# Kernel optimization log

Hardware: AMD Instinct MI355X
Metric: run time of the kernel (lower is better)

The kernel has to match this reference:

```python
import jax, jax.numpy as jnp
import numpy as np

N_HEAD = 16


def setup_inputs() -> dict:
    key = jax.random.key(0)
    ks = jax.random.split(key, 6)
    B, T, H = 4, 2048, 1024
    inp = jax.random.normal(ks[0], (B, T, H), dtype=jnp.float32)
    # padding mask: valid prefix of random length in [T//2, T] per batch row
    lengths = jax.random.randint(ks[1], (B, 1), T // 2, T + 1)
    mask = jnp.arange(T)[None, :] < lengths  # (B, T) bool
    s = 0.02
    w_qkv = jax.random.normal(ks[2], (H, 3 * H), dtype=jnp.float32) * s
    b_qkv = jax.random.normal(ks[3], (3 * H,), dtype=jnp.float32) * s
    w_out = jax.random.normal(ks[4], (H, H), dtype=jnp.float32) * s
    b_out = jax.random.normal(ks[5], (H,), dtype=jnp.float32) * s
    return {"input": inp, "mask": mask, "w_qkv": w_qkv, "b_qkv": b_qkv,
            "w_out": w_out, "b_out": b_out}


def reference(input, mask, w_qkv, b_qkv, w_out, b_out):
    B, T, H = input.shape
    hd = H // N_HEAD
    qkv = input @ w_qkv + b_qkv                       # (B, T, 3H)
    q, k, v = jnp.split(qkv, 3, axis=-1)
    # (B, T, H) -> (B, nh, T, hd)
    q = q.reshape(B, T, N_HEAD, hd).transpose(0, 2, 1, 3)
    k = k.reshape(B, T, N_HEAD, hd).transpose(0, 2, 1, 3)
    v = v.reshape(B, T, N_HEAD, hd).transpose(0, 2, 1, 3)
    scores = jnp.einsum('bhqd,bhkd->bhqk', q, k) / jnp.sqrt(jnp.float32(hd))
    causal = jnp.tril(jnp.ones((T, T), dtype=bool))   # (T, T)
    full_mask = causal[None, None, :, :] & mask[:, None, None, :]  # (B,1,T,T) bcast over heads
    scores = jnp.where(full_mask, scores, -jnp.inf)
    attn = jax.nn.softmax(scores, axis=-1)            # (B, nh, T, T)
    o = jnp.einsum('bhqk,bhkd->bhqd', attn, v)        # (B, nh, T, hd)
    o = o.transpose(0, 2, 1, 3).reshape(B, T, H)
    return o @ w_out + b_out
```

## Files before the change

kernel.cpp:

```cpp
#include <hip/hip_runtime.h>
#include <math.h>

#define B_  4
#define T_  2048
#define H_  1024
#define NH  16
#define HD  64
#define H3  3072

typedef short bf16x8 __attribute__((ext_vector_type(8)));
typedef short bf16x4 __attribute__((ext_vector_type(4)));
typedef float f32x4  __attribute__((ext_vector_type(4)));
typedef float f32x16 __attribute__((ext_vector_type(16)));

#define SC2F 0.18033688011112042f

__device__ __forceinline__ unsigned short f2bf(float f) {
    union { float f; unsigned u; } v; v.f = f;
    unsigned u = v.u;
    unsigned r = (u + 0x7fffu + ((u >> 16) & 1u)) >> 16;
    return (unsigned short)r;
}

__device__ __forceinline__ void gload_lds16(const void* g, void* l) {
    __builtin_amdgcn_global_load_lds(
        (const __attribute__((address_space(1))) unsigned*)g,
        (__attribute__((address_space(3))) unsigned*)l, 16, 0, 0);
}

__device__ __forceinline__ f32x4 mfma_16x16x16_bf16(bf16x4 a, bf16x4 b, f32x4 c) {
#if __has_builtin(__builtin_amdgcn_mfma_f32_16x16x16_bf16)
    return __builtin_amdgcn_mfma_f32_16x16x16_bf16(a, b, c, 0, 0, 0);
#elif __has_builtin(__builtin_amdgcn_mfma_f32_16x16x16bf16_1k)
    return __builtin_amdgcn_mfma_f32_16x16x16bf16_1k(a, b, c, 0, 0, 0);
#else
    f32x4 d;
    asm volatile("v_mfma_f32_16x16x16_bf16 %0, %1, %2, %3"
                 : "=v"(d) : "v"(a), "v"(b), "v"(c));
    return d;
#endif
}

__global__ __launch_bounds__(256) void prep_kernel(
    const float* __restrict__ X, unsigned short* __restrict__ Xbf,
    const float* __restrict__ Wqkv, unsigned short* __restrict__ WqkvT,
    const float* __restrict__ Wout, unsigned short* __restrict__ WoutT)
{
    int bid = blockIdx.x;
    int t = threadIdx.x;
    if (bid < 4096) {
        __shared__ unsigned short tile[32][33];
        int bxx = bid & 127, byy = bid >> 7;
        const float* in;
        unsigned short* out;
        int N, nb;
        if (bxx < 96) { in = Wqkv; out = WqkvT; N = H3; nb = bxx * 32; }
        else          { in = Wout; out = WoutT; N = H_; nb = (bxx - 96) * 32; }
        int kb = byy * 32;
        int tx = t & 31, ty = t >> 5;
        for (int i = 0; i < 32; i += 8)
            tile[ty + i][tx] = f2bf(in[(long)(kb + ty + i) * N + nb + tx]);
        __syncthreads();
        for (int i = 0; i < 32; i += 8)
            out[(long)(nb + ty + i) * H_ + kb + tx] = tile[tx][ty + i];
    } else {
        long u = (long)(bid - 4096) * 256 + t;
#pragma unroll
        for (int j = 0; j < 4; j++) {
            long i = (u + (long)j * 524288) * 4;
            float4 v = *(const float4*)(X + i);
            ushort4 o;
            o.x = f2bf(v.x); o.y = f2bf(v.y); o.z = f2bf(v.z); o.w = f2bf(v.w);
            *(ushort4*)(Xbf + i) = o;
        }
    }
}

__global__ __launch_bounds__(256, 5) void gemm_qkv_kernel(
    const unsigned short* __restrict__ A,
    const unsigned short* __restrict__ Bt,
    const float* __restrict__ bias,
    unsigned short* __restrict__ C,
    unsigned short* __restrict__ Vt)
{
    const int K = H_, N = H3;
    __shared__ unsigned short Asm[128][64];
    __shared__ unsigned short Bsm[128][64];

    int tn = blockIdx.x * 128, tm = blockIdx.y * 128;
    int tid = threadIdx.x;
    int wid = tid >> 6, lane = tid & 63;
    int l31 = lane & 31, lh = lane >> 5;
    int wm = (wid & 1) * 64, wn = (wid >> 1) * 64;

    int rl = lane >> 3;
    int g8 = ((lane & 7) ^ rl) * 8;
    const unsigned short* aP = A  + (long)(tm + wid * 32 + rl) * K + g8;
    const unsigned short* bP = Bt + (long)(tn + wid * 32 + rl) * K + g8;
    int rk = l31 & 7;

    f32x16 acc[2][2] = {};

    for (int k0 = 0; k0 < K; k0 += 64) {
        __syncthreads();
#pragma unroll
        for (int t = 0; t < 4; t++)
            gload_lds16(aP + (long)(t * 8) * K + k0, &Asm[wid * 32 + t * 8][0]);
#pragma unroll
        for (int t = 0; t < 4; t++)
            gload_lds16(bP + (long)(t * 8) * K + k0, &Bsm[wid * 32 + t * 8][0]);
        __syncthreads();

#pragma unroll
        for (int ks = 0; ks < 4; ks++) {
            int pc = ((ks * 2 + lh) ^ rk) * 8;
            bf16x8 af[2], bv[2];
            af[0] = *(const bf16x8*)(&Asm[wm + l31][pc]);
            af[1] = *(const bf16x8*)(&Asm[wm + 32 + l31][pc]);
            bv[0] = *(const bf16x8*)(&Bsm[wn + l31][pc]);
            bv[1] = *(const bf16x8*)(&Bsm[wn + 32 + l31][pc]);
#pragma unroll
            for (int i = 0; i < 2; i++)
#pragma unroll
                for (int j = 0; j < 2; j++)
                    acc[i][j] = __builtin_amdgcn_mfma_f32_32x32x16_bf16(
                        af[i], bv[j], acc[i][j], 0, 0, 0);
        }
    }

    if (tn >= 2 * H_) {
#pragma unroll
        for (int i = 0; i < 2; i++)
#pragma unroll
            for (int j = 0; j < 2; j++) {
                int col = tn + wn + j * 32 + l31;
                float bs = bias[col];
                int feat = col - 2 * H_;
#pragma unroll
                for (int rg = 0; rg < 4; rg++) {
                    int tok0 = tm + wm + i * 32 + rg * 8 + lh * 4;
                    int bb = tok0 >> 11;
                    unsigned d0 = (unsigned)f2bf(acc[i][j][rg * 4 + 0] + bs) |
                                  ((unsigned)f2bf(acc[i][j][rg * 4 + 1] + bs) << 16);
                    unsigned d1 = (unsigned)f2bf(acc[i][j][rg * 4 + 2] + bs) |
                                  ((unsigned)f2bf(acc[i][j][rg * 4 + 3] + bs) << 16);
                    unsigned short* dst = Vt + ((long)(bb * 1024 + feat)) * T_ + (tok0 & (T_ - 1));
                    *(uint2*)dst = make_uint2(d0, d1);
                }
            }
        return;
    }

#pragma unroll
    for (int i = 0; i < 2; i++)
#pragma unroll
        for (int j = 0; j < 2; j++) {
            int col = tn + wn + j * 32 + l31;
            float bs = bias[col];
            bool ks_ = (col >= H_) && (col < 2 * H_);
#pragma unroll
            for (int r = 0; r < 16; r++) {
                int row = tm + wm + i * 32 + (r & 3) + 8 * (r >> 2) + 4 * lh;
                float v = acc[i][j][r] + bs;
                if (ks_) v *= SC2F;
                C[(long)row * N + col] = f2bf(v);
            }
        }
}

template <int TN>
__global__ __launch_bounds__(256) void gemm_kernel(
    const unsigned short* __restrict__ A,
    const unsigned short* __restrict__ Bt,
    const float* __restrict__ bias,
    float* __restrict__ C,
    int M, int N, int K)
{
    __shared__ unsigned short Asm[2][128][64];
    __shared__ unsigned short Bsm[2][TN][64];

    int nbx = gridDim.x;
    int bid = blockIdx.y * nbx + blockIdx.x;
    int cpx = (nbx * gridDim.y) >> 3;
    int lin = (bid & 7) * cpx + (bid >> 3);
    int bx = lin % nbx, by = lin / nbx;

    int tn = bx * TN, tm = by * 128;
    int tid = threadIdx.x;
    int wid = tid >> 6, lane = tid & 63;
    int l31 = lane & 31, lh = lane >> 5;
    int wm = (wid & 1) * 64, wn = (wid >> 1) * (TN / 2);

    int rl = lane >> 3;
    int g8 = ((lane & 7) ^ rl) * 8;
    const unsigned short* aP = A  + (long)(tm + wid * 32 + rl) * K + g8;
    const unsigned short* bP = Bt + (long)(tn + wid * (TN / 4) + rl) * K + g8;
    int rk = l31 & 7;

    f32x16 acc[2][TN / 64] = {};

#pragma unroll
    for (int t = 0; t < 4; t++)
        gload_lds16(aP + (long)(t * 8) * K, &Asm[0][wid * 32 + t * 8][0]);
#pragma unroll
    for (int t = 0; t < TN / 32; t++)
        gload_lds16(bP + (long)(t * 8) * K, &Bsm[0][wid * (TN / 4) + t * 8][0]);

    int cur = 0;
    for (int k0 = 0; k0 < K; k0 += 64) {
        __syncthreads();
        if (k0 + 64 < K) {
#pragma unroll
            for (int t = 0; t < 4; t++)
                gload_lds16(aP + (long)(t * 8) * K + k0 + 64, &Asm[cur ^ 1][wid * 32 + t * 8][0]);
#pragma unroll
            for (int t = 0; t < TN / 32; t++)
                gload_lds16(bP + (long)(t * 8) * K + k0 + 64, &Bsm[cur ^ 1][wid * (TN / 4) + t * 8][0]);
        }
#pragma unroll
        for (int ks = 0; ks < 4; ks++) {
            int pc = ((ks * 2 + lh) ^ rk) * 8;
            bf16x8 af[2], bv[TN / 64];
            af[0] = *(const bf16x8*)(&Asm[cur][wm + l31][pc]);
            af[1] = *(const bf16x8*)(&Asm[cur][wm + 32 + l31][pc]);
#pragma unroll
            for (int j = 0; j < TN / 64; j++)
                bv[j] = *(const bf16x8*)(&Bsm[cur][wn + j * 32 + l31][pc]);
#pragma unroll
            for (int i = 0; i < 2; i++)
#pragma unroll
                for (int j = 0; j < TN / 64; j++)
                    acc[i][j] = __builtin_amdgcn_mfma_f32_32x32x16_bf16(
                        af[i], bv[j], acc[i][j], 0, 0, 0);
        }
        cur ^= 1;
    }

#pragma unroll
    for (int i = 0; i < 2; i++)
#pragma unroll
        for (int j = 0; j < TN / 64; j++) {
            int col = tn + wn + j * 32 + l31;
            float bs = bias[col];
#pragma unroll
            for (int r = 0; r < 16; r++) {
                int row = tm + wm + i * 32 + (r & 3) + 8 * (r >> 2) + 4 * lh;
                C[(long)row * N + col] = acc[i][j][r] + bs;
            }
        }
}

__global__ __launch_bounds__(256) void attn_kernel(
    const unsigned short* __restrict__ QKV,
    const unsigned short* __restrict__ Vt,
    const void* __restrict__ mask,
    unsigned short* __restrict__ O)
{
    int idx = blockIdx.x;
    int bh = idx & 63;
    int qt = 15 - (idx >> 6);
    int b = bh >> 4, h = bh & 15;
    int q0 = qt * 128;

    int tid = threadIdx.x;
    int wid = tid >> 6, lane = tid & 63, quad = lane >> 4, lr = lane & 15;
    int quad4 = quad * 4;

    int len;
    {
        const unsigned* mu = (const unsigned*)mask;
        bool is_byte = (mu[0] == 0x01010101u);
        int cnt = 0;
        if (is_byte) {
            const unsigned char* m8 = (const unsigned char*)mask;
            for (int i = lane; i < T_; i += 64) cnt += (m8[b * T_ + i] != 0);
        } else {
            const unsigned* m32 = (const unsigned*)mask;
            for (int i = lane; i < T_; i += 64) cnt += (m32[b * T_ + i] != 0);
        }
        cnt += __shfl_xor(cnt, 1);  cnt += __shfl_xor(cnt, 2);
        cnt += __shfl_xor(cnt, 4);  cnt += __shfl_xor(cnt, 8);
        cnt += __shfl_xor(cnt, 16); cnt += __shfl_xor(cnt, 32);
        len = cnt;
    }

    __shared__ __align__(16) unsigned short SH[16384];
    unsigned short (*Kd)[64][64] = (unsigned short (*)[64][64])(&SH[0]);
    unsigned short (*Vd)[64][64] = (unsigned short (*)[64][64])(&SH[8192]);

    const long qkv_base = (long)b * T_ * H3;

    bf16x8 qf[2][2];
#pragma unroll
    for (int nq = 0; nq < 2; nq++)
#pragma unroll
        for (int ks = 0; ks < 2; ks++)
            qf[nq][ks] = *(const bf16x8*)(QKV + qkv_base +
                (long)(q0 + wid * 32 + nq * 16 + lr) * H3 + h * HD + ks * 32 + quad * 8);

    int rl = lane >> 3;
    int g8 = ((lane & 7) ^ rl) * 8;
    const unsigned short* kB = QKV + qkv_base + (long)(wid * 16 + rl) * H3 + H_ + h * HD + g8;
    const unsigned short* vB = Vt + (long)(bh * 64 + wid * 16 + rl) * T_ + g8;

    f32x4 lacc[2] = {};
    f32x4 Oacc[4][2] = {};

    int kmax = min(q0 + 127, len - 1);
    int n_kt = (kmax >> 6) + 1;
    int q_wave_lo = q0 + wid * 32;
    int qwl_u = __builtin_amdgcn_readfirstlane(q_wave_lo);
    int q_wave_hi = qwl_u + 31;
    int bnd_[2] = { min(q_wave_lo + lr, len - 1),
                    min(q_wave_lo + 16 + lr, len - 1) };
    int rk = lr & 7;

    const short oneb = (short)0x3F80;
    bf16x4 vones = { oneb, oneb, oneb, oneb };

#pragma unroll
    for (int t = 0; t < 2; t++) {
        gload_lds16(kB + (long)(t * 8) * H3, &Kd[0][wid * 16 + t * 8][0]);
        gload_lds16(vB + (long)(t * 8) * T_, &Vd[0][wid * 16 + t * 8][0]);
    }

    for (int kt = 0; kt < n_kt; kt++) {
        int cur = kt & 1;
        __syncthreads();

        if (kt + 1 < n_kt) {
            long koff = (long)((kt + 1) * 64) * H3;
            int voff = (kt + 1) * 64;
#pragma unroll
            for (int t = 0; t < 2; t++) {
                gload_lds16(kB + koff + (long)(t * 8) * H3, &Kd[cur ^ 1][wid * 16 + t * 8][0]);
                gload_lds16(vB + (long)(t * 8) * T_ + voff, &Vd[cur ^ 1][wid * 16 + t * 8][0]);
            }
        }

        int k_lo = kt * 64;
        if (k_lo > q_wave_hi || k_lo >= len) continue;

        int mt_hi = min(q_wave_hi, len - 1);
        int nmt = min(4, ((mt_hi - k_lo) >> 4) + 1);
        nmt = __builtin_amdgcn_readfirstlane(nmt);

        f32x4 Sacc[4][2] = {};
        __builtin_amdgcn_s_setprio(1);
#pragma unroll
        for (int mt = 0; mt < 4; mt++) {
            if (mt >= nmt) continue;
#pragma unroll
            for (int ks = 0; ks < 2; ks++) {
                bf16x8 kf = *(const bf16x8*)(&Kd[cur][mt * 16 + lr][((ks * 4 + quad) ^ rk) * 8]);
                Sacc[mt][0] = __builtin_amdgcn_mfma_f32_16x16x32_bf16(kf, qf[0][ks], Sacc[mt][0], 0, 0, 0);
                Sacc[mt][1] = __builtin_amdgcn_mfma_f32_16x16x32_bf16(kf, qf[1][ks], Sacc[mt][1], 0, 0, 0);
            }
        }
        __builtin_amdgcn_s_setprio(0);

        unsigned pkk[4][2][2];
#pragma unroll
        for (int mt = 0; mt < 4; mt++) {
            if (mt >= nmt) continue;
            int kb0 = k_lo + mt * 16;
            int kbl = kb0 + quad4;
#pragma unroll
            for (int nq = 0; nq < 2; nq++) {
                float p[4];
                if (kb0 + 15 <= qwl_u + nq * 16 && kb0 + 15 < len) {
#pragma unroll
                    for (int r = 0; r < 4; r++)
                        p[r] = __builtin_amdgcn_exp2f(Sacc[mt][nq][r]);
                } else {
                    int dlt = bnd_[nq] - kbl;
#pragma unroll
                    for (int r = 0; r < 4; r++) {
                        float s = (r <= dlt) ? Sacc[mt][nq][r] : -INFINITY;
                        p[r] = __builtin_amdgcn_exp2f(s);
                    }
                }
                pkk[mt][nq][0] = __builtin_amdgcn_perm(__float_as_uint(p[1]), __float_as_uint(p[0]), 0x07060302);
                pkk[mt][nq][1] = __builtin_amdgcn_perm(__float_as_uint(p[3]), __float_as_uint(p[2]), 0x07060302);
            }
        }

        __builtin_amdgcn_s_setprio(1);
#pragma unroll
        for (int mt = 0; mt < 4; mt++) {
            if (mt >= nmt) continue;
            union { unsigned u[2]; bf16x4 v; } bu[2];
            bu[0].u[0] = pkk[mt][0][0]; bu[0].u[1] = pkk[mt][0][1];
            bu[1].u[0] = pkk[mt][1][0]; bu[1].u[1] = pkk[mt][1][1];
            lacc[0] = mfma_16x16x16_bf16(vones, bu[0].v, lacc[0]);
            lacc[1] = mfma_16x16x16_bf16(vones, bu[1].v, lacc[1]);
#pragma unroll
            for (int md = 0; md < 4; md++) {
                bf16x4 vf = *(const bf16x4*)(&Vd[cur][md * 16 + lr]
                    [((mt * 2 + (quad >> 1)) ^ rk) * 8 + (quad & 1) * 4]);
                Oacc[md][0] = mfma_16x16x16_bf16(vf, bu[0].v, Oacc[md][0]);
                Oacc[md][1] = mfma_16x16x16_bf16(vf, bu[1].v, Oacc[md][1]);
            }
        }
        __builtin_amdgcn_s_setprio(0);
    }

    __syncthreads();
    {
        unsigned short (*Es)[68] = (unsigned short (*)[68])(&SH[0]);
        float inv[2] = { 1.f / lacc[0][0], 1.f / lacc[1][0] };
#pragma unroll
        for (int nq = 0; nq < 2; nq++)
#pragma unroll
            for (int md = 0; md < 4; md++)
#pragma unroll
                for (int rp = 0; rp < 2; rp++) {
                    float e0 = Oacc[md][nq][rp * 2]     * inv[nq];
                    float e1 = Oacc[md][nq][rp * 2 + 1] * inv[nq];
                    unsigned w = __builtin_amdgcn_perm(__float_as_uint(e1), __float_as_uint(e0), 0x07060302);
                    *(unsigned*)(&Es[wid * 32 + nq * 16 + lr][md * 16 + quad * 4 + rp * 2]) = w;
                }
        __asm__ volatile("s_waitcnt lgkmcnt(0)" ::: "memory");
        int row = lane >> 1, cb = (lane & 1) * 32;
        long tok = (long)b * T_ + q0 + wid * 32 + row;
#pragma unroll
        for (int i = 0; i < 4; i++) {
            float4 v = *(const float4*)(&Es[wid * 32 + row][cb + i * 8]);
            *(float4*)(&O[tok * H_ + h * HD + cb + i * 8]) = v;
        }
    }
}

extern "C" void kernel_launch(void* const* d_in, const int* in_sizes, int n_in,
                              void* d_out, int out_size, void* d_ws, size_t ws_size,
                              hipStream_t stream) {
    const float* X    = (const float*)d_in[0];
    const void*  mask = d_in[1];
    const float* Wqkv = (const float*)d_in[2];
    const float* bqkv = (const float*)d_in[3];
    const float* Wout = (const float*)d_in[4];
    const float* bout = (const float*)d_in[5];

    char* ws = (char*)d_ws;
    unsigned short* WqkvT = (unsigned short*)(ws + 256);
    unsigned short* WoutT = WqkvT + (long)H3 * H_;
    unsigned short* QKV   = WoutT + (long)H_ * H_;
    unsigned short* Xbf   = QKV + (long)B_ * T_ * H3;
    unsigned short* Vt    = Xbf + (long)B_ * T_ * H_;
    unsigned short* Obf   = Xbf;

    const int M = B_ * T_;

    prep_kernel<<<6144, 256, 0, stream>>>(X, Xbf, Wqkv, WqkvT, Wout, WoutT);
    gemm_qkv_kernel<<<dim3(H3 / 128, M / 128), 256, 0, stream>>>(
        Xbf, WqkvT, bqkv, QKV, Vt);
    attn_kernel<<<B_ * NH * (T_ / 128), 256, 0, stream>>>(QKV, Vt, mask, Obf);
    gemm_kernel<64><<<dim3(H_ / 64, M / 128), 256, 0, stream>>>(
        Obf, WoutT, bout, (float*)d_out, M, H_, H_);
}
```

Measured before the change: 264.0 us.

## Split long causal attention query tiles across two KV halves with combine pass

Adds a split-KV attention kernel. The upper eight query tiles, which have the longest causal key ranges, are each split into two blocks that cover half the key tiles and write unnormalized fp32 partial outputs and row sums to workspace. A combine kernel then sums the halves, normalizes, and writes bf16 output. The aim is to balance the work per block and raise parallelism (1536 blocks instead of 1024), at the cost of an extra launch plus partial-result writes and reads. It relies on a fixed softmax offset with no running max, so the partial sums combine by simple addition. A fallback to the original kernel is kept if the workspace is too small.

```diff
diff --git a/kernel.cpp b/kernel.cpp
--- a/kernel.cpp
+++ b/kernel.cpp
@@ -250,6 +250,255 @@
         }
 }
 
+__global__ __launch_bounds__(256) void attn_split_kernel(
+    const unsigned short* __restrict__ QKV,
+    const unsigned short* __restrict__ Vt,
+    const void* __restrict__ mask,
+    unsigned short* __restrict__ O,
+    float* __restrict__ Part,
+    float* __restrict__ Lp)
+{
+    int idx = blockIdx.x;
+    int bh = idx & 63;
+    int b = bh >> 4, h = bh & 15;
+
+    int tid = threadIdx.x;
+    int wid = tid >> 6, lane = tid & 63, quad = lane >> 4, lr = lane & 15;
+    int quad4 = quad * 4;
+
+    int len;
+    {
+        const unsigned* mu = (const unsigned*)mask;
+        bool is_byte = (mu[0] == 0x01010101u);
+        int cnt = 0;
+        if (is_byte) {
+            const unsigned char* m8 = (const unsigned char*)mask;
+            for (int i = lane; i < T_; i += 64) cnt += (m8[b * T_ + i] != 0);
+        } else {
+            const unsigned* m32 = (const unsigned*)mask;
+            for (int i = lane; i < T_; i += 64) cnt += (m32[b * T_ + i] != 0);
+        }
+        cnt += __shfl_xor(cnt, 1);  cnt += __shfl_xor(cnt, 2);
+        cnt += __shfl_xor(cnt, 4);  cnt += __shfl_xor(cnt, 8);
+        cnt += __shfl_xor(cnt, 16); cnt += __shfl_xor(cnt, 32);
+        len = cnt;
+    }
+
+    int qt, kb0, kb1, unit;
+    bool spl;
+    if (idx < 1024) {
+        int u = idx >> 6;
+        qt = 15 - (u >> 1);
+        int half = u & 1;
+        int kmax = min(qt * 128 + 127, len - 1);
+        int n_kt = (kmax >> 6) + 1;
+        int nh = n_kt >> 1;
+        kb0 = half ? nh : 0;
+        kb1 = half ? n_kt : nh;
+        unit = (bh * 8 + (qt - 8)) * 2 + half;
+        spl = true;
+    } else {
+        int u = (idx - 1024) >> 6;
+        qt = 7 - u;
+        int kmax = min(qt * 128 + 127, len - 1);
+        kb0 = 0;
+        kb1 = (kmax >> 6) + 1;
+        unit = 0;
+        spl = false;
+    }
+    int q0 = qt * 128;
+
+    __shared__ __align__(16) unsigned short SH[16384];
+    unsigned short (*Kd)[64][64] = (unsigned short (*)[64][64])(&SH[0]);
+    unsigned short (*Vd)[64][64] = (unsigned short (*)[64][64])(&SH[8192]);
+
+    const long qkv_base = (long)b * T_ * H3;
+
+    bf16x8 qf[2][2];
+#pragma unroll
+    for (int nq = 0; nq < 2; nq++)
+#pragma unroll
+        for (int ks = 0; ks < 2; ks++)
+            qf[nq][ks] = *(const bf16x8*)(QKV + qkv_base +
+                (long)(q0 + wid * 32 + nq * 16 + lr) * H3 + h * HD + ks * 32 + quad * 8);
+
+    int rl = lane >> 3;
+    int g8 = ((lane & 7) ^ rl) * 8;
+    const unsigned short* kB = QKV + qkv_base + (long)(wid * 16 + rl) * H3 + H_ + h * HD + g8;
+    const unsigned short* vB = Vt + (long)(bh * 64 + wid * 16 + rl) * T_ + g8;
+
+    f32x4 lacc[2] = {};
+    f32x4 Oacc[4][2] = {};
+
+    int q_wave_lo = q0 + wid * 32;
+    int qwl_u = __builtin_amdgcn_readfirstlane(q_wave_lo);
+    int q_wave_hi = qwl_u + 31;
+    int bnd_[2] = { min(q_wave_lo + lr, len - 1),
+                    min(q_wave_lo + 16 + lr, len - 1) };
+    int rk = lr & 7;
+
+    const short oneb = (short)0x3F80;
+    bf16x4 vones = { oneb, oneb, oneb, oneb };
+
+#pragma unroll
+    for (int t = 0; t < 2; t++) {
+        gload_lds16(kB + (long)(kb0 * 64) * H3 + (long)(t * 8) * H3, &Kd[0][wid * 16 + t * 8][0]);
+        gload_lds16(vB + (long)(t * 8) * T_ + kb0 * 64, &Vd[0][wid * 16 + t * 8][0]);
+    }
+
+    for (int kt = kb0; kt < kb1; kt++) {
+        int cur = (kt - kb0) & 1;
+        __syncthreads();
+
+        if (kt + 1 < kb1) {
+            long koff = (long)((kt + 1) * 64) * H3;
+            int voff = (kt + 1) * 64;
+#pragma unroll
+            for (int t = 0; t < 2; t++) {
+                gload_lds16(kB + koff + (long)(t * 8) * H3, &Kd[cur ^ 1][wid * 16 + t * 8][0]);
+                gload_lds16(vB + (long)(t * 8) * T_ + voff, &Vd[cur ^ 1][wid * 16 + t * 8][0]);
+            }
+        }
+
+        int k_lo = kt * 64;
+        if (k_lo > q_wave_hi || k_lo >= len) continue;
+
+        int mt_hi = min(q_wave_hi, len - 1);
+        int nmt = min(4, ((mt_hi - k_lo) >> 4) + 1);
+        nmt = __builtin_amdgcn_readfirstlane(nmt);
+
+        f32x4 Sacc[4][2] = {};
+        __builtin_amdgcn_s_setprio(1);
+#pragma unroll
+        for (int mt = 0; mt < 4; mt++) {
+            if (mt >= nmt) continue;
+#pragma unroll
+            for (int ks = 0; ks < 2; ks++) {
+                bf16x8 kf = *(const bf16x8*)(&Kd[cur][mt * 16 + lr][((ks * 4 + quad) ^ rk) * 8]);
+                Sacc[mt][0] = __builtin_amdgcn_mfma_f32_16x16x32_bf16(kf, qf[0][ks], Sacc[mt][0], 0, 0, 0);
+                Sacc[mt][1] = __builtin_amdgcn_mfma_f32_16x16x32_bf16(kf, qf[1][ks], Sacc[mt][1], 0, 0, 0);
+            }
+        }
+        __builtin_amdgcn_s_setprio(0);
+
+        unsigned pkk[4][2][2];
+#pragma unroll
+        for (int mt = 0; mt < 4; mt++) {
+            if (mt >= nmt) continue;
+            int kb0_ = k_lo + mt * 16;
+            int kbl = kb0_ + quad4;
+#pragma unroll
+            for (int nq = 0; nq < 2; nq++) {
+                float p[4];
+                if (kb0_ + 15 <= qwl_u + nq * 16 && kb0_ + 15 < len) {
+#pragma unroll
+                    for (int r = 0; r < 4; r++)
+                        p[r] = __builtin_amdgcn_exp2f(Sacc[mt][nq][r]);
+                } else {
+                    int dlt = bnd_[nq] - kbl;
+#pragma unroll
+                    for (int r = 0; r < 4; r++) {
+                        float s = (r <= dlt) ? Sacc[mt][nq][r] : -INFINITY;
+                        p[r] = __builtin_amdgcn_exp2f(s);
+                    }
+                }
+                pkk[mt][nq][0] = __builtin_amdgcn_perm(__float_as_uint(p[1]), __float_as_uint(p[0]), 0x07060302);
+                pkk[mt][nq][1] = __builtin_amdgcn_perm(__float_as_uint(p[3]), __float_as_uint(p[2]), 0x07060302);
+            }
+        }
+
+        __builtin_amdgcn_s_setprio(1);
+#pragma unroll
+        for (int mt = 0; mt < 4; mt++) {
+            if (mt >= nmt) continue;
+            union { unsigned u[2]; bf16x4 v; } bu[2];
+            bu[0].u[0] = pkk[mt][0][0]; bu[0].u[1] = pkk[mt][0][1];
+            bu[1].u[0] = pkk[mt][1][0]; bu[1].u[1] = pkk[mt][1][1];
+            lacc[0] = mfma_16x16x16_bf16(vones, bu[0].v, lacc[0]);
+            lacc[1] = mfma_16x16x16_bf16(vones, bu[1].v, lacc[1]);
+#pragma unroll
+            for (int md = 0; md < 4; md++) {
+                bf16x4 vf = *(const bf16x4*)(&Vd[cur][md * 16 + lr]
+                    [((mt * 2 + (quad >> 1)) ^ rk) * 8 + (quad & 1) * 4]);
+                Oacc[md][0] = mfma_16x16x16_bf16(vf, bu[0].v, Oacc[md][0]);
+                Oacc[md][1] = mfma_16x16x16_bf16(vf, bu[1].v, Oacc[md][1]);
+            }
+        }
+        __builtin_amdgcn_s_setprio(0);
+    }
+
+    __syncthreads();
+
+    if (spl) {
+        float* Pb = Part + (long)unit * 8192;
+#pragma unroll
+        for (int nq = 0; nq < 2; nq++) {
+            int row = wid * 32 + nq * 16 + lr;
+#pragma unroll
+            for (int md = 0; md < 4; md++)
+                *(f32x4*)(Pb + row * 64 + md * 16 + quad4) = Oacc[md][nq];
+            if (quad == 0)
+                Lp[unit * 128 + row] = lacc[nq][0];
+        }
+        return;
+    }
+
+    {
+        unsigned short (*Es)[68] = (unsigned short (*)[68])(&SH[0]);
+        float inv[2] = { 1.f / lacc[0][0], 1.f / lacc[1][0] };
+#pragma unroll
+        for (int nq = 0; nq < 2; nq++)
+#pragma unroll
+            for (int md = 0; md < 4; md++)
+#pragma unroll
+                for (int rp = 0; rp < 2; rp++) {
+                    float e0 = Oacc[md][nq][rp * 2]     * inv[nq];
+                    float e1 = Oacc[md][nq][rp * 2 + 1] * inv[nq];
+                    unsigned w = __builtin_amdgcn_perm(__float_as_uint(e1), __float_as_uint(e0), 0x07060302);
+                    *(unsigned*)(&Es[wid * 32 + nq * 16 + lr][md * 16 + quad * 4 + rp * 2]) = w;
+                }
+        __asm__ volatile("s_waitcnt lgkmcnt(0)" ::: "memory");
+        int row = lane >> 1, cb = (lane & 1) * 32;
+        long tok = (long)b * T_ + q0 + wid * 32 + row;
+#pragma unroll
+        for (int i = 0; i < 4; i++) {
+            float4 v = *(const float4*)(&Es[wid * 32 + row][cb + i * 8]);
+            *(float4*)(&O[tok * H_ + h * HD + cb + i * 8]) = v;
+        }
+    }
+}
+
+__global__ __launch_bounds__(256) void combine_kernel(
+    const float* __restrict__ Part, const float* __restrict__ Lp,
+    unsigned short* __restrict__ O)
+{
+    int idx = blockIdx.x;
+    int bh = idx >> 3, qm = idx & 7;
+    int b = bh >> 4, h = bh & 15;
+    int qt = qm + 8;
+    long u0 = ((long)bh * 8 + qm) * 2;
+    const float* P0 = Part + u0 * 8192;
+    const float* P1 = P0 + 8192;
+    const float* L0 = Lp + u0 * 128;
+    const float* L1 = L0 + 128;
+    int t = threadIdx.x;
+#pragma unroll
+    for (int i = 0; i < 8; i++) {
+        int e4 = i * 256 + t;
+        int row = e4 >> 4;
+        int f4 = e4 & 15;
+        f32x4 a = *(const f32x4*)(P0 + (long)e4 * 4);
+        f32x4 c = *(const f32x4*)(P1 + (long)e4 * 4);
+        float inv = 1.f / (L0[row] + L1[row]);
+        unsigned w0 = (unsigned)f2bf((a[0] + c[0]) * inv) |
+                      ((unsigned)f2bf((a[1] + c[1]) * inv) << 16);
+        unsigned w1 = (unsigned)f2bf((a[2] + c[2]) * inv) |
+                      ((unsigned)f2bf((a[3] + c[3]) * inv) << 16);
+        long tok = (long)b * T_ + qt * 128 + row;
+        *(uint2*)(O + tok * H_ + h * HD + f4 * 4) = make_uint2(w0, w1);
+    }
+}
+
 __global__ __launch_bounds__(256) void attn_kernel(
     const unsigned short* __restrict__ QKV,
     const unsigned short* __restrict__ Vt,
@@ -449,12 +698,23 @@
     unsigned short* Vt    = Xbf + (long)B_ * T_ * H_;
     unsigned short* Obf   = Xbf;
 
+    const long part_off = 256 + (long)H3 * H_ * 2 + (long)H_ * H_ * 2
+                        + (long)B_ * T_ * H3 * 2 + 2 * (long)B_ * T_ * H_ * 2;
+    float* Part = (float*)(ws + part_off);
+    float* Lp   = (float*)(ws + part_off + 33554432);
+    const size_t ws_need = (size_t)part_off + 33554432 + 524288;
+
     const int M = B_ * T_;
 
     prep_kernel<<<6144, 256, 0, stream>>>(X, Xbf, Wqkv, WqkvT, Wout, WoutT);
     gemm_qkv_kernel<<<dim3(H3 / 128, M / 128), 256, 0, stream>>>(
         Xbf, WqkvT, bqkv, QKV, Vt);
-    attn_kernel<<<B_ * NH * (T_ / 128), 256, 0, stream>>>(QKV, Vt, mask, Obf);
+    if (ws_size >= ws_need) {
+        attn_split_kernel<<<1536, 256, 0, stream>>>(QKV, Vt, mask, Obf, Part, Lp);
+        combine_kernel<<<512, 256, 0, stream>>>(Part, Lp, Obf);
+    } else {
+        attn_kernel<<<B_ * NH * (T_ / 128), 256, 0, stream>>>(QKV, Vt, mask, Obf);
+    }
     gemm_kernel<64><<<dim3(H_ / 64, M / 128), 256, 0, stream>>>(
         Obf, WoutT, bout, (float*)d_out, M, H_, H_);
 }
```

Measured after the change: 304.0 us. 1.15x slower.
